# Kernel optimization log

Measured on AMD Instinct MI355X. Metric: run time of the kernel, lower is better.

## Reference

```python
import jax, jax.numpy as jnp
import numpy as np

EPS = 1e-5

def _conv(x, w, pad):
    return jax.lax.conv_general_dilated(x, w, (1, 1), pad,
        dimension_numbers=('NCHW', 'OIHW', 'NCHW'))

def _bn_relu(y, g, b):
    # training-mode BatchNorm2d: stats over (N, H, W) per channel
    mean = jnp.mean(y, axis=(0, 2, 3), keepdims=True)
    var = jnp.var(y, axis=(0, 2, 3), keepdims=True)
    yhat = (y - mean) * jax.lax.rsqrt(var + EPS)
    return jax.nn.relu(yhat * g[None, :, None, None] + b[None, :, None, None])


def setup_inputs() -> dict:
    key = jax.random.key(0)
    ks = jax.random.split(key, 12)
    B, Cin, H, W = 4, 256, 64, 64
    Ci = Cin // 4          # inter_channels = 64
    Cq = Ci // 8           # PAM q/k dim = 8
    Cout = 256
    s = 0.05
    return {
        'x':    jax.random.normal(ks[0], (B, Cin, H, W), jnp.float32),
        'w1':   jax.random.normal(ks[1], (Ci, Cin, 3, 3), jnp.float32) * s,
        'bn_g': jnp.ones((Ci,), jnp.float32),
        'bn_b': jnp.zeros((Ci,), jnp.float32),
        'wq':   jax.random.normal(ks[2], (Cq, Ci, 1, 1), jnp.float32) * s,
        'bq':   jax.random.normal(ks[3], (Cq,), jnp.float32) * s,
        'wk':   jax.random.normal(ks[4], (Cq, Ci, 1, 1), jnp.float32) * s,
        'bk':   jax.random.normal(ks[5], (Cq,), jnp.float32) * s,
        'wv':   jax.random.normal(ks[6], (Ci, Ci, 1, 1), jnp.float32) * s,
        'bv':   jax.random.normal(ks[7], (Ci,), jnp.float32) * s,
        'gamma_pam': jnp.float32(0.5) * jnp.ones((1,), jnp.float32),
        'gamma_cam': jnp.float32(0.5) * jnp.ones((1,), jnp.float32),
        'w2':   jax.random.normal(ks[8], (Ci, Ci, 3, 3), jnp.float32) * s,
        'w8':   jax.random.normal(ks[9], (Cout, Ci, 1, 1), jnp.float32) * s,
        'b8':   jax.random.normal(ks[10], (Cout,), jnp.float32) * s,
    }


def reference(x, w1, bn_g, bn_b, wq, bq, wk, bk, wv, bv,
              gamma_pam, gamma_cam, w2, w8, b8):
    B, _, H, W = x.shape
    N = H * W

    # feat1 = relu(bn1(conv1(x))); feat2 is the identical computation -> reuse
    feat1 = _bn_relu(_conv(x, w1, 'SAME'), bn_g, bn_b)   # [B, Ci, H, W]
    Ci = feat1.shape[1]

    # ---- PAM (position attention) ----
    q = _conv(feat1, wq, 'VALID') + bq[None, :, None, None]   # [B, Cq, H, W]
    k = _conv(feat1, wk, 'VALID') + bk[None, :, None, None]
    v = _conv(feat1, wv, 'VALID') + bv[None, :, None, None]   # [B, Ci, H, W]
    qf = q.reshape(B, -1, N)
    kf = k.reshape(B, -1, N)
    vf = v.reshape(B, Ci, N)
    energy = jnp.einsum('bdi,bdj->bij', qf, kf)               # [B, N, N]
    attn = jax.nn.softmax(energy, axis=-1)
    pam = jnp.einsum('bcj,bij->bci', vf, attn).reshape(B, Ci, H, W)
    sa_feat = gamma_pam[0] * pam + feat1

    sa_conv = _bn_relu(_conv(sa_feat, w2, 'SAME'), bn_g, bn_b)

    # ---- CAM (channel attention) ----
    f = feat1.reshape(B, Ci, N)
    ce = jnp.einsum('bcn,bdn->bcd', f, f)                     # [B, Ci, Ci]
    ce_new = jnp.max(ce, axis=-1, keepdims=True) - ce
    cattn = jax.nn.softmax(ce_new, axis=-1)
    cam = jnp.einsum('bcd,bdn->bcn', cattn, f).reshape(B, Ci, H, W)
    sc_feat = gamma_cam[0] * cam + feat1

    sc_conv = _bn_relu(_conv(sc_feat, w2, 'SAME'), bn_g, bn_b)

    feat_sum = sa_conv + sc_conv
    # conv8: Dropout2d (identity at inference) + 1x1 conv
    out = _conv(feat_sum, w8, 'VALID') + b8[None, :, None, None]
    return out
```

## Files before the change

### kernel.cpp

```cpp
#include <hip/hip_runtime.h>
#include <hip/hip_bf16.h>

#define BB   4
#define CIN  256
#define CI   64
#define COUT 256
#define NPIX 4096
#define LOG2E 1.44269504088896340736f

#define B_Y1V    0x0000000u
#define B_FEAT1  0x0400000u
#define B_SA     0x0800000u
#define B_Y2     0x0C00000u
#define B_SACONV 0x1000000u
#define B_Q      0x1400000u
#define B_K      0x1480000u
#define B_ST     0x15A0000u
#define B_CATT   0x15B1000u
#define B_WP1    0x15C1000u
#define B_WP2    0x1610000u
#define B_PL     0x1630000u
#define B_W8P    0x1640000u
#define B_WQKV   0x1648000u
#define B_BALL   0x164B000u

typedef __attribute__((ext_vector_type(8))) short bf16x8;
typedef __attribute__((ext_vector_type(4))) short bf16x4;
typedef __attribute__((ext_vector_type(4))) float f32x4;

__device__ __forceinline__ short f2bs(float f) {
    union { float f; unsigned u; } c; c.f = f;
    unsigned r = c.u + 0x7FFFu + ((c.u >> 16) & 1u);
    return (short)(r >> 16);
}
__device__ __forceinline__ float bs2f(unsigned short s) {
    union { unsigned u; float f; } c; c.u = ((unsigned)s) << 16;
    return c.f;
}
__device__ __forceinline__ int swz(int wp) { return (wp ^ (wp >> 2)) & 3; }


__device__ __forceinline__ void weights_body(const float* __restrict__ w1,
                                             const float* __restrict__ w2,
                                             const float* __restrict__ w8,
                                             const float* wq, const float* bq,
                                             const float* wk, const float* bk,
                                             const float* wv, const float* bv,
                                             short* wp1, short* wp2, short* w8p,
                                             short* wall, float* ball,
                                             float* st, float* pl, int blk, int t) {
    if (blk < 576) {
        int idx = blk * 256 + t;
        if (idx < 147456) {
            int cil = idx & 31, co = (idx >> 5) & 63;
            int rest = idx >> 11, tap = rest % 9, ch = rest / 9;
            wp1[idx] = f2bs(w1[co * CIN * 9 + (ch * 32 + cil) * 9 + tap]);
        }
    } else if (blk < 720) {
        int idx = (blk - 576) * 256 + t;
        if (idx < 36864) {
            int cil = idx & 31, co = (idx >> 5) & 63;
            int rest = idx >> 11, tap = rest % 9, ch = rest / 9;
            wp2[idx] = f2bs(w2[co * CI * 9 + (ch * 32 + cil) * 9 + tap]);
        }
    } else if (blk < 784) {
        int idx = (blk - 720) * 256 + t;
        w8p[idx] = f2bs(w8[idx]);
    } else if (blk < 804) {
        int idx = (blk - 784) * 256 + t;
        if (idx < 5120) {
            int co = idx >> 6, ci = idx & 63;
            float v;
            if (co < 8)       v = wq[co * 64 + ci] * LOG2E;
            else if (co < 16) v = wk[(co - 8) * 64 + ci];
            else              v = wv[(co - 16) * 64 + ci];
            wall[idx] = f2bs(v);
        }
        if (idx < 80) {
            float v;
            if (idx < 8)       v = bq[idx] * LOG2E;
            else if (idx < 16) v = bk[idx - 8];
            else               v = bv[idx - 16];
            ball[idx] = v;
        }
    } else if (blk < 806) {
        int idx = (blk - 804) * 256 + t;
        if (idx < 384) st[idx] = 0.f;
    } else {
        int idx = (blk - 806) * 256 + t;
        pl[idx] = 0.f;
    }
}

template<int NCH>
__device__ __forceinline__ void prep_body(const float* __restrict__ in,
                                          short* __restrict__ out, int blk, int t) {
    __shared__ short tl[4][64][34];
    int hq = blk & 15;
    int ch = (blk >> 4) % NCH;
    int b  = blk / (16 * NCH);
    const int CINT = NCH * 32;

    #pragma unroll
    for (int i = 0; i < 32; ++i) {
        int idx = i * 256 + t;
        int w = idx & 63, hh = (idx >> 6) & 3, ci = idx >> 8;
        float v = in[((size_t)(b * CINT + ch * 32 + ci)) * NPIX + (hq * 4 + hh) * 64 + w];
        tl[hh][w][ci] = f2bs(v);
    }
    __syncthreads();
    unsigned* outu = (unsigned*)(out + (((size_t)(b * NCH + ch)) * NPIX + hq * 4 * 64) * 32);
    #pragma unroll
    for (int i = 0; i < 16; ++i) {
        int j = i * 256 + t;
        int cip = j & 15, w = (j >> 4) & 63, hh = j >> 10;
        unsigned v = *(unsigned*)&tl[hh][w][2 * cip];
        outu[(size_t)(hh * 64 + w) * 16 + cip] = v;
    }
}

__global__ __launch_bounds__(256) void k_prepw(const float* __restrict__ x,
                                               const float* w1, const float* w2, const float* w8,
                                               const float* wq, const float* bq,
                                               const float* wk, const float* bk,
                                               const float* wv, const float* bv,
                                               short* xprep,
                                               short* wp1, short* wp2, short* w8p,
                                               short* wall, float* ball,
                                               float* st, float* pl) {
    int blk = blockIdx.x, t = threadIdx.x;
    if (blk < 512) prep_body<8>(x, xprep, blk, t);
    else weights_body(w1, w2, w8, wq, bq, wk, bk, wv, bv,
                      wp1, wp2, w8p, wall, ball, st, pl, blk - 512, t);
}

__device__ __forceinline__ void pamprep_body(const short* __restrict__ po,
                                             const float* __restrict__ pl_acc,
                                             const float* __restrict__ feat1,
                                             const float* __restrict__ gp,
                                             short* __restrict__ out, int blk, int t) {
    __shared__ short tl[4][64][34];
    int hq = blk & 15;
    int ch = (blk >> 4) & 1;
    int b  = blk >> 5;
    float g = gp[0];

    #pragma unroll
    for (int i = 0; i < 32; ++i) {
        int idx = i * 256 + t;
        int w = idx & 63, hh = (idx >> 6) & 3, ci = idx >> 8;
        int pix = (hq * 4 + hh) * 64 + w;
        size_t o = ((size_t)(b * 64 + ch * 32 + ci)) * NPIX + pix;
        float s = bs2f((unsigned short)po[o])
                + bs2f((unsigned short)po[o + 1048576])
                + bs2f((unsigned short)po[o + 2097152])
                + bs2f((unsigned short)po[o + 3145728]);
        float v = feat1[o] + g * s / pl_acc[b * NPIX + pix];
        tl[hh][w][ci] = f2bs(v);
    }
    __syncthreads();
    unsigned* outu = (unsigned*)(out + (((size_t)(b * 2 + ch)) * NPIX + hq * 4 * 64) * 32);
    #pragma unroll
    for (int i = 0; i < 16; ++i) {
        int j = i * 256 + t;
        int cip = j & 15, w = (j >> 4) & 63, hh = j >> 10;
        unsigned v = *(unsigned*)&tl[hh][w][2 * cip];
        outu[(size_t)(hh * 64 + w) * 16 + cip] = v;
    }
}

__global__ __launch_bounds__(256) void k_preppam(const float* __restrict__ scfeat,
                                                 short* __restrict__ sprep_sc,
                                                 const short* __restrict__ po,
                                                 const float* __restrict__ pl_acc,
                                                 const float* __restrict__ feat1,
                                                 const float* __restrict__ gp,
                                                 short* __restrict__ saprep) {
    int blk = blockIdx.x, t = threadIdx.x;
    if (blk < 128) prep_body<2>(scfeat, sprep_sc, blk, t);
    else pamprep_body(po, pl_acc, feat1, gp, saprep, blk - 128, t);
}

template<int NCH>
__device__ __forceinline__ void conv_body(const short* __restrict__ xprep,
                                          const short* __restrict__ wp,
                                          float* __restrict__ y0,
                                          float* __restrict__ y1,
                                          int blk, int t) {
    __shared__ __align__(16) short xl[3][66][32];
    int lane = t & 63, wv = t >> 6;
    int ks = blk >> 8;
    int b = (blk >> 6) & 3, h = blk & 63;
    int g = lane >> 4, n16 = lane & 15;
    constexpr int NH = NCH / 2;
    int c0 = ks * NH;

    if (t < 24) {
        int r = t >> 3, cc = ((t >> 2) & 1) ? 65 : 0, u = t & 3;
        bf16x8 z = {};
        *(bf16x8*)&xl[r][cc][u * 8] = z;
    }

    f32x4 acc[4];
    #pragma unroll
    for (int i = 0; i < 4; ++i) acc[i] = (f32x4){0.f, 0.f, 0.f, 0.f};

    int sw = t >> 2, su = t & 3;
    int spu = su ^ swz(sw + 1);

    for (int ch = c0; ch < c0 + NH; ++ch) {
        __syncthreads();
        #pragma unroll
        for (int r = 0; r < 3; ++r) {
            int hh = h + r - 1;
            bf16x8 v = {};
            if (hh >= 0 && hh < 64)
                v = *(const bf16x8*)(xprep + (((size_t)(b * NCH + ch)) * 64 + hh) * 64 * 32 + sw * 32 + su * 8);
            *(bf16x8*)&xl[r][sw + 1][spu * 8] = v;
        }
        __syncthreads();

        const short* wbase = wp + ((size_t)(ch * 9)) * 64 * 32;
        #pragma unroll
        for (int tap = 0; tap < 9; ++tap) {
            int kr = tap / 3, kc = tap % 3;
            bf16x8 a = *(const bf16x8*)(wbase + ((size_t)(tap * 64 + wv * 16 + n16)) * 32 + g * 8);
            #pragma unroll
            for (int nt = 0; nt < 4; ++nt) {
                int wpix = nt * 16 + n16 + kc;
                int pu = g ^ swz(wpix);
                bf16x8 bx = *(const bf16x8*)&xl[kr][wpix][pu * 8];
                acc[nt] = __builtin_amdgcn_mfma_f32_16x16x32_bf16(a, bx, acc[nt], 0, 0, 0);
            }
        }
    }

    float* y = ks ? y1 : y0;
    #pragma unroll
    for (int nt = 0; nt < 4; ++nt) {
        #pragma unroll
        for (int r = 0; r < 4; ++r) {
            int co = wv * 16 + g * 4 + r;
            y[((size_t)(b * CI + co)) * NPIX + h * 64 + nt * 16 + n16] = acc[nt][r];
        }
    }
}

template<int NCH>
__global__ __launch_bounds__(256) void k_convmfma(const short* __restrict__ xprep,
                                                  const short* __restrict__ wp,
                                                  float* __restrict__ y0,
                                                  float* __restrict__ y1) {
    conv_body<NCH>(xprep, wp, y0, y1, blockIdx.x, threadIdx.x);
}

__global__ __launch_bounds__(256) void k_conv2x(const short* __restrict__ inA,
                                                const short* __restrict__ inB,
                                                const short* __restrict__ wp,
                                                float* a0, float* a1,
                                                float* b0, float* b1) {
    int blk = blockIdx.x;
    int w = blk >> 9;
    conv_body<2>(w ? inB : inA, wp, w ? b0 : a0, w ? b1 : a1, blk & 511, threadIdx.x);
}

__device__ __forceinline__ void bnstats_body(const float* __restrict__ y0,
                                             const float* __restrict__ y1,
                                             float* stats, int blk, int t) {
    int c = blk >> 2, b = blk & 3;
    size_t base = ((size_t)(b * 64 + c)) * NPIX;
    float s = 0.f, sq = 0.f;
    for (int i = t; i < NPIX; i += 256) {
        float v = y0[base + i] + y1[base + i];
        s += v; sq += v * v;
    }
    __shared__ float rs[8];
    for (int o = 32; o; o >>= 1) { s += __shfl_down(s, o); sq += __shfl_down(sq, o); }
    if ((t & 63) == 0) { rs[t >> 6] = s; rs[4 + (t >> 6)] = sq; }
    __syncthreads();
    if (t == 0) {
        atomicAdd(&stats[c], rs[0] + rs[1] + rs[2] + rs[3]);
        atomicAdd(&stats[64 + c], rs[4] + rs[5] + rs[6] + rs[7]);
    }
}

__global__ __launch_bounds__(256) void k_bnstats(const float* y0, const float* y1, float* stats) {
    bnstats_body(y0, y1, stats, blockIdx.x, threadIdx.x);
}
__global__ __launch_bounds__(256) void k_bnstats2x(const float* a0, const float* a1,
                                                   const float* b0, const float* b1,
                                                   float* sta, float* stb) {
    int blk = blockIdx.x;
    int w = blk >> 8;
    bnstats_body(w ? b0 : a0, w ? b1 : a1, w ? stb : sta, blk & 255, threadIdx.x);
}

__device__ __forceinline__ void bnapply_body(const float* y0, const float* y1,
                                             const float* stats, const float* g,
                                             const float* bta, float* out, int i) {
    int c = (i >> 12) & 63;
    float mean = stats[c] * (1.f / 16384.f);
    float var = stats[64 + c] * (1.f / 16384.f) - mean * mean;
    float rs = rsqrtf(var + 1e-5f);
    float v = (y0[i] + y1[i] - mean) * rs * g[c] + bta[c];
    out[i] = v > 0.f ? v : 0.f;
}

__global__ __launch_bounds__(256) void k_bnapply2(const float* y0, const float* y1,
                                                  const float* stats, const float* g,
                                                  const float* bta, float* out) {
    bnapply_body(y0, y1, stats, g, bta, out, blockIdx.x * 256 + threadIdx.x);
}
__global__ __launch_bounds__(256) void k_bnapply2x(const float* a0, const float* a1,
                                                   const float* b0, const float* b1,
                                                   const float* sta, const float* stb,
                                                   const float* g, const float* bta,
                                                   float* oa, float* ob) {
    int blk = blockIdx.x;
    int w = blk >> 12;
    int i = (blk & 4095) * 256 + threadIdx.x;
    bnapply_body(w ? b0 : a0, w ? b1 : a1, w ? stb : sta, g, bta, w ? ob : oa, i);
}

__device__ __forceinline__ void qkv_body(const float* __restrict__ feat1,
                                         const short* __restrict__ wall,
                                         const float* __restrict__ ball,
                                         short* __restrict__ q,
                                         short* __restrict__ k,
                                         short* __restrict__ v, int blk, int t) {
    __shared__ __align__(16) short fl[64][64];
    int lane = t & 63, wv = t >> 6;
    int h = blk & 63, b = blk >> 6;
    int n16 = lane & 15, g = lane >> 4;

    {
        int n = t & 63, ug2 = t >> 6;
        const float* fp = feat1 + ((size_t)b * CI) * NPIX + h * 64 + n;
        #pragma unroll
        for (int uu = 0; uu < 2; ++uu) {
            int u = ug2 + uu * 4;
            int ci0 = u * 8;
            short tmp[8];
            #pragma unroll
            for (int j = 0; j < 8; ++j) tmp[j] = f2bs(fp[(size_t)(ci0 + j) * NPIX]);
            int phys = u ^ (n & 7);
            *(bf16x8*)&fl[n][phys * 8] = *(bf16x8*)tmp;
        }
    }
    __syncthreads();

    f32x4 acc[4];
    #pragma unroll
    for (int i = 0; i < 4; ++i) acc[i] = (f32x4){0.f, 0.f, 0.f, 0.f};
    f32x4 acc4 = (f32x4){0.f, 0.f, 0.f, 0.f};

    #pragma unroll
    for (int kc = 0; kc < 2; ++kc) {
        bf16x8 a = *(const bf16x8*)&wall[(size_t)(wv * 16 + n16) * 64 + kc * 32 + g * 8];
        bf16x8 a4 = *(const bf16x8*)&wall[(size_t)(64 + n16) * 64 + kc * 32 + g * 8];
        #pragma unroll
        for (int nt = 0; nt < 4; ++nt) {
            int n = nt * 16 + n16;
            int phys = (kc * 4 + g) ^ (n & 7);
            bf16x8 bx = *(const bf16x8*)&fl[n][phys * 8];
            acc[nt] = __builtin_amdgcn_mfma_f32_16x16x32_bf16(a, bx, acc[nt], 0, 0, 0);
            if (nt == wv) acc4 = __builtin_amdgcn_mfma_f32_16x16x32_bf16(a4, bx, acc4, 0, 0, 0);
        }
    }

    #pragma unroll
    for (int nt = 0; nt < 4; ++nt) {
        int pix = h * 64 + nt * 16 + n16;
        #pragma unroll
        for (int r = 0; r < 4; ++r) {
            int co = wv * 16 + g * 4 + r;
            short val = f2bs(acc[nt][r] + ball[co]);
            if (co < 8)       q[((size_t)(b * 8 + co)) * NPIX + pix] = val;
            else if (co < 16) k[((size_t)(b * 8 + co - 8)) * NPIX + pix] = val;
            else              v[((size_t)(b * 64 + co - 16)) * NPIX + pix] = val;
        }
    }
    {
        int pix = h * 64 + wv * 16 + n16;
        #pragma unroll
        for (int r = 0; r < 4; ++r) {
            int co = 64 + g * 4 + r;
            v[((size_t)(b * 64 + co - 16)) * NPIX + pix] = f2bs(acc4[r] + ball[co]);
        }
    }
}

__device__ __forceinline__ void gram_body(const float* __restrict__ f,
                                          float* __restrict__ gp, int blk, int t) {
    __shared__ __align__(16) float fl[64 * 68];
    int b = blk >> 6, nc = blk & 63;
    int n0 = nc * 64;
    int c = t & 63, dg = t >> 6;
    float acc[16];
    #pragma unroll
    for (int i = 0; i < 16; ++i) acc[i] = 0.f;
    for (int idx = t; idx < 4096; idx += 256) {
        int cc = idx >> 6, nn = idx & 63;
        fl[nn * 68 + cc] = f[((size_t)b * 64 + cc) * NPIX + n0 + nn];
    }
    __syncthreads();
    for (int nn = 0; nn < 64; ++nn) {
        float fc = fl[nn * 68 + c];
        const float4* fd = (const float4*)(fl + nn * 68 + dg * 16);
        #pragma unroll
        for (int k4 = 0; k4 < 4; ++k4) {
            float4 vv = fd[k4];
            acc[k4 * 4 + 0] += fc * vv.x;
            acc[k4 * 4 + 1] += fc * vv.y;
            acc[k4 * 4 + 2] += fc * vv.z;
            acc[k4 * 4 + 3] += fc * vv.w;
        }
    }
    float* dst = gp + (size_t)nc * 16384 + ((size_t)b * 64 + c) * 64 + dg * 16;
    #pragma unroll
    for (int kk = 0; kk < 16; ++kk) dst[kk] = acc[kk];
}

__global__ __launch_bounds__(256) void k_qkvgram(const float* __restrict__ feat1,
                                                 const short* __restrict__ wall,
                                                 const float* __restrict__ ball,
                                                 short* q, short* k, short* v,
                                                 float* gp) {
    int blk = blockIdx.x, t = threadIdx.x;
    if (blk < 256) qkv_body(feat1, wall, ball, q, k, v, blk, t);
    else gram_body(feat1, gp, blk - 256, t);
}

__global__ __launch_bounds__(256) void k_pampart(const short* __restrict__ q,
                                                 const short* __restrict__ k,
                                                 const short* __restrict__ v,
                                                 short* __restrict__ po,
                                                 float* __restrict__ pl_acc) {
    __shared__ short kl[128][20];
    __shared__ __align__(16) short pl[64][128];

    int t = threadIdx.x;
    int lane = t & 63, w = t >> 6;
    int blk = blockIdx.x;
    int jc = blk >> 8, b = (blk >> 6) & 3, ic = blk & 63;
    int i0 = ic * 64;
    int n16 = lane & 15, g = lane >> 4;
    int key = n16 & 7;

    const short* qb = q + (size_t)b * 8 * NPIX;
    const short* kb = k + (size_t)b * 8 * NPIX;
    const short* vb = v + (size_t)b * 64 * NPIX;

    #pragma unroll
    for (int i = 0; i < 2; ++i) {
        int idx = i * 256 + t;
        int jj = idx & 127, dz = 8 + ((idx >> 7) << 1);
        *(unsigned*)&kl[jj][dz] = 0u;
    }

    bf16x8 aq = {};
    if (lane < 16) {
        int irow = i0 + w * 16 + lane;
        #pragma unroll
        for (int e = 0; e < 8; ++e) aq[e] = qb[(size_t)e * NPIX + irow];
    }

    f32x4 acc[4];
    #pragma unroll
    for (int i = 0; i < 4; ++i) acc[i] = (f32x4){0.f, 0.f, 0.f, 0.f};
    float lacc = 0.f;
    const f32x4 zz = {0.f, 0.f, 0.f, 0.f};

    for (int ro = 0; ro < 8; ++ro) {
        int j0 = jc * 1024 + ro * 128;
        #pragma unroll
        for (int i = 0; i < 2; ++i) {
            int idx = i * 256 + t;
            int jj = idx & 127, dp2 = idx >> 7;
            unsigned lo = (unsigned short)kb[(size_t)(dp2 * 2) * NPIX + j0 + jj];
            unsigned hi = (unsigned short)kb[(size_t)(dp2 * 2 + 1) * NPIX + j0 + jj];
            *(unsigned*)&kl[jj][dp2 * 2] = lo | (hi << 16);
        }
        bf16x8 av[4];
        #pragma unroll
        for (int ks = 0; ks < 4; ++ks)
            av[ks] = *(const bf16x8*)&vb[(size_t)(w * 16 + n16) * NPIX + j0 + ks * 32 + g * 8];
        __syncthreads();

        __builtin_amdgcn_s_setprio(1);
        #pragma unroll
        for (int jsub = 0; jsub < 8; ++jsub) {
            bf16x8 bk = {};
            if (lane < 32) {
                bf16x4 lo = *(const bf16x4*)&kl[jsub * 16 + n16][g * 8];
                bf16x4 hi = *(const bf16x4*)&kl[jsub * 16 + n16][g * 8 + 4];
                bk = __builtin_shufflevector(lo, hi, 0, 1, 2, 3, 4, 5, 6, 7);
            }
            f32x4 s = __builtin_amdgcn_mfma_f32_16x16x32_bf16(bk, aq, zz, 0, 0, 0);
            float e0 = exp2f(s[0]), e1 = exp2f(s[1]), e2 = exp2f(s[2]), e3 = exp2f(s[3]);
            lacc += (e0 + e1) + (e2 + e3);
            bf16x4 pk = { f2bs(e0), f2bs(e1), f2bs(e2), f2bs(e3) };
            int uw = (jsub * 2 + (g >> 1)) ^ key;
            *(bf16x4*)&pl[w * 16 + n16][uw * 8 + (g & 1) * 4] = pk;
        }
        __builtin_amdgcn_s_setprio(0);
        __syncthreads();

        __builtin_amdgcn_s_setprio(1);
        #pragma unroll
        for (int isub = 0; isub < 4; ++isub) {
            #pragma unroll
            for (int ks = 0; ks < 4; ++ks) {
                int ur = (ks * 4 + g) ^ key;
                bf16x8 bp = *(const bf16x8*)&pl[isub * 16 + n16][ur * 8];
                acc[isub] = __builtin_amdgcn_mfma_f32_16x16x32_bf16(av[ks], bp, acc[isub], 0, 0, 0);
            }
        }
        __builtin_amdgcn_s_setprio(0);
        __syncthreads();
    }

    {
        float lv = lacc;
        lv += __shfl_xor(lv, 16);
        lv += __shfl_xor(lv, 32);
        if (lane < 16)
            atomicAdd(&pl_acc[b * NPIX + i0 + w * 16 + lane], lv);
    }

    #pragma unroll
    for (int isub = 0; isub < 4; ++isub) {
        #pragma unroll
        for (int r = 0; r < 4; ++r) {
            int c = w * 16 + g * 4 + r;
            size_t o = ((size_t)((jc * BB + b) * 64 + c)) * NPIX + i0 + isub * 16 + n16;
            po[o] = f2bs(acc[isub][r]);
        }
    }
}

__global__ void k_camsm2(const float* __restrict__ gp, float* __restrict__ cattn) {
    int row = blockIdx.x;
    int d = threadIdx.x;
    float v = 0.f;
    #pragma unroll 8
    for (int p = 0; p < 64; ++p) v += gp[(size_t)p * 16384 + row * 64 + d];
    float mn = v;
    for (int s = 32; s; s >>= 1) mn = fminf(mn, __shfl_xor(mn, s));
    float e = exp2f((mn - v) * LOG2E);
    float sum = e;
    for (int s = 32; s; s >>= 1) sum += __shfl_xor(sum, s);
    cattn[(size_t)row * 64 + d] = e / sum;
}

__global__ __launch_bounds__(256) void k_cam(const float* __restrict__ cattn,
                                             const float* __restrict__ f,
                                             const float* __restrict__ gcp,
                                             float* __restrict__ sc) {
    __shared__ __align__(16) float Al[64 * 68];
    __shared__ float fl[64 * 64];
    int blk = blockIdx.x;
    int b = blk >> 6, nc = blk & 63;
    int n0 = nc * 64;
    int t = threadIdx.x;
    int nl = t & 63, cg = t >> 6;
    for (int idx = t; idx < 4096; idx += 256) {
        int cc = idx >> 6, dd = idx & 63;
        Al[dd * 68 + cc] = cattn[((size_t)b * 64 + cc) * 64 + dd];
    }
    for (int idx = t; idx < 4096; idx += 256) {
        int dd = idx >> 6, nn = idx & 63;
        fl[dd * 64 + nn] = f[((size_t)b * 64 + dd) * NPIX + n0 + nn];
    }
    __syncthreads();
    float acc[16];
    #pragma unroll
    for (int i = 0; i < 16; ++i) acc[i] = 0.f;
    for (int d = 0; d < 64; ++d) {
        float fv = fl[d * 64 + nl];
        const float4* A4 = (const float4*)(Al + d * 68 + cg * 16);
        #pragma unroll
        for (int k4 = 0; k4 < 4; ++k4) {
            float4 a = A4[k4];
            acc[k4 * 4 + 0] += a.x * fv;
            acc[k4 * 4 + 1] += a.y * fv;
            acc[k4 * 4 + 2] += a.z * fv;
            acc[k4 * 4 + 3] += a.w * fv;
        }
    }
    float g = gcp[0];
    #pragma unroll
    for (int kk = 0; kk < 16; ++kk) {
        int c = cg * 16 + kk;
        size_t o = ((size_t)b * 64 + c) * NPIX + n0 + nl;
        sc[o] = g * acc[kk] + f[o];
    }
}

__global__ __launch_bounds__(256) void k_finalmfma(const float* __restrict__ sa,
                                                   const float* __restrict__ sc,
                                                   const short* __restrict__ w8p,
                                                   const float* __restrict__ b8,
                                                   float* __restrict__ out) {
    __shared__ __align__(16) short fl[64][64];
    int t = threadIdx.x;
    int lane = t & 63, wv = t >> 6;
    int blk = blockIdx.x;
    int h = blk & 63, b = (blk >> 6) & 3, cq = blk >> 8;
    int n16 = lane & 15, g = lane >> 4;

    {
        int n = t & 63, ug2 = t >> 6;
        const float* sap = sa + ((size_t)b * CI) * NPIX + h * 64 + n;
        const float* scp = sc + ((size_t)b * CI) * NPIX + h * 64 + n;
        #pragma unroll
        for (int uu = 0; uu < 2; ++uu) {
            int u = ug2 + uu * 4;
            int ci0 = u * 8;
            short tmp[8];
            #pragma unroll
            for (int j = 0; j < 8; ++j) {
                size_t o = (size_t)(ci0 + j) * NPIX;
                tmp[j] = f2bs(sap[o] + scp[o]);
            }
            int phys = u ^ (n & 7);
            *(bf16x8*)&fl[n][phys * 8] = *(bf16x8*)tmp;
        }
    }
    __syncthreads();

    f32x4 acc[4];
    #pragma unroll
    for (int i = 0; i < 4; ++i) acc[i] = (f32x4){0.f, 0.f, 0.f, 0.f};
    int cobase = cq * 64 + wv * 16;

    #pragma unroll
    for (int kc = 0; kc < 2; ++kc) {
        bf16x8 a = *(const bf16x8*)&w8p[(size_t)(cobase + n16) * 64 + kc * 32 + g * 8];
        #pragma unroll
        for (int nt = 0; nt < 4; ++nt) {
            int n = nt * 16 + n16;
            int phys = (kc * 4 + g) ^ (n & 7);
            bf16x8 bx = *(const bf16x8*)&fl[n][phys * 8];
            acc[nt] = __builtin_amdgcn_mfma_f32_16x16x32_bf16(a, bx, acc[nt], 0, 0, 0);
        }
    }

    #pragma unroll
    for (int nt = 0; nt < 4; ++nt) {
        #pragma unroll
        for (int r = 0; r < 4; ++r) {
            int co = cobase + g * 4 + r;
            out[((size_t)(b * COUT + co)) * NPIX + h * 64 + nt * 16 + n16] = acc[nt][r] + b8[co];
        }
    }
}

extern "C" void kernel_launch(void* const* d_in, const int* in_sizes, int n_in,
                              void* d_out, int out_size, void* d_ws, size_t ws_size,
                              hipStream_t stream) {
    (void)in_sizes; (void)n_in; (void)out_size; (void)ws_size;
    const float* x    = (const float*)d_in[0];
    const float* w1   = (const float*)d_in[1];
    const float* bng  = (const float*)d_in[2];
    const float* bnb  = (const float*)d_in[3];
    const float* wq   = (const float*)d_in[4];
    const float* bq   = (const float*)d_in[5];
    const float* wk   = (const float*)d_in[6];
    const float* bk   = (const float*)d_in[7];
    const float* wv   = (const float*)d_in[8];
    const float* bv   = (const float*)d_in[9];
    const float* gpam = (const float*)d_in[10];
    const float* gcam = (const float*)d_in[11];
    const float* w2   = (const float*)d_in[12];
    const float* w8   = (const float*)d_in[13];
    const float* b8   = (const float*)d_in[14];
    float* out = (float*)d_out;

    char* WB = (char*)d_ws;
    float* fC1P0   = (float*)(WB + B_Y1V);
    float* fC1P1   = (float*)(WB + B_SACONV);
    float* fGP     = (float*)(WB + B_SACONV);
    short* fV      = (short*)(WB + B_Y1V);
    short* fSPREPSC= (short*)(WB + B_Y1V + 0x200000);
    short* fSAPREP = (short*)(WB + B_Y1V);
    float* fFEAT1  = (float*)(WB + B_FEAT1);
    short* fXPREP  = (short*)(WB + B_SA);
    float* fSCFEAT = (float*)(WB + B_SA);
    float* fC2B1   = (float*)(WB + B_SA);
    short* fPO     = (short*)(WB + B_Y2);
    float* fC2A0   = (float*)(WB + B_Y2);
    float* fC2B0   = (float*)(WB + B_FEAT1);
    float* fC2A1   = (float*)(WB + B_SACONV);
    short* fQ      = (short*)(WB + B_Q);
    short* fK      = (short*)(WB + B_K);
    float* fST     = (float*)(WB + B_ST);
    float* fST2a   = fST + 128;
    float* fST2b   = fST + 256;
    float* fCATT   = (float*)(WB + B_CATT);
    short* fWP1    = (short*)(WB + B_WP1);
    short* fWP2    = (short*)(WB + B_WP2);
    float* fPL     = (float*)(WB + B_PL);
    short* fW8P    = (short*)(WB + B_W8P);
    short* fWQKV   = (short*)(WB + B_WQKV);
    float* fBALL   = (float*)(WB + B_BALL);

    k_prepw<<<1382, 256, 0, stream>>>(x, w1, w2, w8, wq, bq, wk, bk, wv, bv,
                                      fXPREP, fWP1, fWP2, fW8P, fWQKV, fBALL, fST, fPL);

    k_convmfma<8><<<512, 256, 0, stream>>>(fXPREP, fWP1, fC1P0, fC1P1);
    k_bnstats<<<256, 256, 0, stream>>>(fC1P0, fC1P1, fST);
    k_bnapply2<<<4096, 256, 0, stream>>>(fC1P0, fC1P1, fST, bng, bnb, fFEAT1);

    k_qkvgram<<<512, 256, 0, stream>>>(fFEAT1, fWQKV, fBALL, fQ, fK, fV, fGP);
    k_camsm2<<<256, 64, 0, stream>>>(fGP, fCATT);

    k_pampart<<<1024, 256, 0, stream>>>(fQ, fK, fV, fPO, fPL);
    k_cam<<<256, 256, 0, stream>>>(fCATT, fFEAT1, gcam, fSCFEAT);
    k_preppam<<<256, 256, 0, stream>>>(fSCFEAT, fSPREPSC, fPO, fPL, fFEAT1, gpam, fSAPREP);

    k_conv2x<<<1024, 256, 0, stream>>>(fSAPREP, fSPREPSC, fWP2, fC2A0, fC2A1, fC2B0, fC2B1);
    k_bnstats2x<<<512, 256, 0, stream>>>(fC2A0, fC2A1, fC2B0, fC2B1, fST2a, fST2b);
    k_bnapply2x<<<8192, 256, 0, stream>>>(fC2A0, fC2A1, fC2B0, fC2B1, fST2a, fST2b,
                                          bng, bnb, fC2A1, fC2B1);

    k_finalmfma<<<1024, 256, 0, stream>>>(fC2A1, fC2B1, fW8P, b8, out);
}
```

Baseline: 136.4 us.

## Fuse CAM matmul with bf16 conv-input prep and split BN stats across more blocks

The CAM attention product now writes the gamma-scaled residual directly in the packed bf16 layout that the second conv consumes. It is merged into one launch with the PAM prep, which removes the fp32 sc_feat round trip and one kernel launch. Separately, the BN statistics kernels split each channel/batch plane into four chunks, giving four times as many blocks. The cost is four times as many atomic adds, plus a change in the floating-point summation order.

```diff
diff --git a/kernel.cpp b/kernel.cpp
--- a/kernel.cpp
+++ b/kernel.cpp
@@ -169,16 +169,61 @@
     }
 }
 
-__global__ __launch_bounds__(256) void k_preppam(const float* __restrict__ scfeat,
-                                                 short* __restrict__ sprep_sc,
-                                                 const short* __restrict__ po,
-                                                 const float* __restrict__ pl_acc,
-                                                 const float* __restrict__ feat1,
-                                                 const float* __restrict__ gp,
-                                                 short* __restrict__ saprep) {
+__device__ __forceinline__ void camprep_body(const float* __restrict__ cattn,
+                                             const float* __restrict__ f,
+                                             const float* __restrict__ gcp,
+                                             short* __restrict__ out, int blk, int t) {
+    __shared__ __align__(16) float Al[64 * 68];
+    __shared__ float fl[64 * 64];
+    int b = blk >> 6, nc = blk & 63;
+    int n0 = nc * 64;
+    int nl = t & 63, cg = t >> 6;
+    for (int idx = t; idx < 4096; idx += 256) {
+        int cc = idx >> 6, dd = idx & 63;
+        Al[dd * 68 + cc] = cattn[((size_t)b * 64 + cc) * 64 + dd];
+    }
+    for (int idx = t; idx < 4096; idx += 256) {
+        int dd = idx >> 6, nn = idx & 63;
+        fl[dd * 64 + nn] = f[((size_t)b * 64 + dd) * NPIX + n0 + nn];
+    }
+    __syncthreads();
+    float acc[16];
+    #pragma unroll
+    for (int i = 0; i < 16; ++i) acc[i] = 0.f;
+    for (int d = 0; d < 64; ++d) {
+        float fv = fl[d * 64 + nl];
+        const float4* A4 = (const float4*)(Al + d * 68 + cg * 16);
+        #pragma unroll
+        for (int k4 = 0; k4 < 4; ++k4) {
+            float4 a = A4[k4];
+            acc[k4 * 4 + 0] += a.x * fv;
+            acc[k4 * 4 + 1] += a.y * fv;
+            acc[k4 * 4 + 2] += a.z * fv;
+            acc[k4 * 4 + 3] += a.w * fv;
+        }
+    }
+    float g = gcp[0];
+    int pix = n0 + nl;
+    unsigned* du = (unsigned*)out + ((size_t)(b * 2 + (cg >> 1)) * NPIX + pix) * 16 + (cg & 1) * 8;
+    #pragma unroll
+    for (int m = 0; m < 8; ++m) {
+        float v0 = g * acc[2 * m]     + fl[(cg * 16 + 2 * m) * 64 + nl];
+        float v1 = g * acc[2 * m + 1] + fl[(cg * 16 + 2 * m + 1) * 64 + nl];
+        du[m] = (unsigned)(unsigned short)f2bs(v0) | ((unsigned)(unsigned short)f2bs(v1) << 16);
+    }
+}
+
+__global__ __launch_bounds__(256) void k_campam(const float* __restrict__ cattn,
+                                                const float* __restrict__ feat1,
+                                                const float* __restrict__ gcp,
+                                                short* __restrict__ sprep_sc,
+                                                const short* __restrict__ po,
+                                                const float* __restrict__ pl_acc,
+                                                const float* __restrict__ gpam,
+                                                short* __restrict__ saprep) {
     int blk = blockIdx.x, t = threadIdx.x;
-    if (blk < 128) prep_body<2>(scfeat, sprep_sc, blk, t);
-    else pamprep_body(po, pl_acc, feat1, gp, saprep, blk - 128, t);
+    if (blk < 256) camprep_body(cattn, feat1, gcp, sprep_sc, blk, t);
+    else pamprep_body(po, pl_acc, feat1, gpam, saprep, blk - 256, t);
 }
 
 template<int NCH>
@@ -267,11 +312,14 @@
 __device__ __forceinline__ void bnstats_body(const float* __restrict__ y0,
                                              const float* __restrict__ y1,
                                              float* stats, int blk, int t) {
-    int c = blk >> 2, b = blk & 3;
-    size_t base = ((size_t)(b * 64 + c)) * NPIX;
+    int pc = blk & 3;
+    int cb = blk >> 2;
+    int c = cb >> 2, b = cb & 3;
+    size_t base = ((size_t)(b * 64 + c)) * NPIX + pc * 1024;
     float s = 0.f, sq = 0.f;
-    for (int i = t; i < NPIX; i += 256) {
-        float v = y0[base + i] + y1[base + i];
+    #pragma unroll
+    for (int i = 0; i < 4; ++i) {
+        float v = y0[base + i * 256 + t] + y1[base + i * 256 + t];
         s += v; sq += v * v;
     }
     __shared__ float rs[8];
@@ -291,8 +339,8 @@
                                                    const float* b0, const float* b1,
                                                    float* sta, float* stb) {
     int blk = blockIdx.x;
-    int w = blk >> 8;
-    bnstats_body(w ? b0 : a0, w ? b1 : a1, w ? stb : sta, blk & 255, threadIdx.x);
+    int w = blk >> 10;
+    bnstats_body(w ? b0 : a0, w ? b1 : a1, w ? stb : sta, blk & 1023, threadIdx.x);
 }
 
 __device__ __forceinline__ void bnapply_body(const float* y0, const float* y1,
@@ -551,50 +599,6 @@
     float sum = e;
     for (int s = 32; s; s >>= 1) sum += __shfl_xor(sum, s);
     cattn[(size_t)row * 64 + d] = e / sum;
-}
-
-__global__ __launch_bounds__(256) void k_cam(const float* __restrict__ cattn,
-                                             const float* __restrict__ f,
-                                             const float* __restrict__ gcp,
-                                             float* __restrict__ sc) {
-    __shared__ __align__(16) float Al[64 * 68];
-    __shared__ float fl[64 * 64];
-    int blk = blockIdx.x;
-    int b = blk >> 6, nc = blk & 63;
-    int n0 = nc * 64;
-    int t = threadIdx.x;
-    int nl = t & 63, cg = t >> 6;
-    for (int idx = t; idx < 4096; idx += 256) {
-        int cc = idx >> 6, dd = idx & 63;
-        Al[dd * 68 + cc] = cattn[((size_t)b * 64 + cc) * 64 + dd];
-    }
-    for (int idx = t; idx < 4096; idx += 256) {
-        int dd = idx >> 6, nn = idx & 63;
-        fl[dd * 64 + nn] = f[((size_t)b * 64 + dd) * NPIX + n0 + nn];
-    }
-    __syncthreads();
-    float acc[16];
-    #pragma unroll
-    for (int i = 0; i < 16; ++i) acc[i] = 0.f;
-    for (int d = 0; d < 64; ++d) {
-        float fv = fl[d * 64 + nl];
-        const float4* A4 = (const float4*)(Al + d * 68 + cg * 16);
-        #pragma unroll
-        for (int k4 = 0; k4 < 4; ++k4) {
-            float4 a = A4[k4];
-            acc[k4 * 4 + 0] += a.x * fv;
-            acc[k4 * 4 + 1] += a.y * fv;
-            acc[k4 * 4 + 2] += a.z * fv;
-            acc[k4 * 4 + 3] += a.w * fv;
-        }
-    }
-    float g = gcp[0];
-    #pragma unroll
-    for (int kk = 0; kk < 16; ++kk) {
-        int c = cg * 16 + kk;
-        size_t o = ((size_t)b * 64 + c) * NPIX + n0 + nl;
-        sc[o] = g * acc[kk] + f[o];
-    }
 }
 
 __global__ __launch_bounds__(256) void k_finalmfma(const float* __restrict__ sa,
@@ -686,7 +690,6 @@
     short* fSAPREP = (short*)(WB + B_Y1V);
     float* fFEAT1  = (float*)(WB + B_FEAT1);
     short* fXPREP  = (short*)(WB + B_SA);
-    float* fSCFEAT = (float*)(WB + B_SA);
     float* fC2B1   = (float*)(WB + B_SA);
     short* fPO     = (short*)(WB + B_Y2);
     float* fC2A0   = (float*)(WB + B_Y2);
@@ -709,18 +712,17 @@
                                       fXPREP, fWP1, fWP2, fW8P, fWQKV, fBALL, fST, fPL);
 
     k_convmfma<8><<<512, 256, 0, stream>>>(fXPREP, fWP1, fC1P0, fC1P1);
-    k_bnstats<<<256, 256, 0, stream>>>(fC1P0, fC1P1, fST);
+    k_bnstats<<<1024, 256, 0, stream>>>(fC1P0, fC1P1, fST);
     k_bnapply2<<<4096, 256, 0, stream>>>(fC1P0, fC1P1, fST, bng, bnb, fFEAT1);
 
     k_qkvgram<<<512, 256, 0, stream>>>(fFEAT1, fWQKV, fBALL, fQ, fK, fV, fGP);
     k_camsm2<<<256, 64, 0, stream>>>(fGP, fCATT);
 
     k_pampart<<<1024, 256, 0, stream>>>(fQ, fK, fV, fPO, fPL);
-    k_cam<<<256, 256, 0, stream>>>(fCATT, fFEAT1, gcam, fSCFEAT);
-    k_preppam<<<256, 256, 0, stream>>>(fSCFEAT, fSPREPSC, fPO, fPL, fFEAT1, gpam, fSAPREP);
+    k_campam<<<384, 256, 0, stream>>>(fCATT, fFEAT1, gcam, fSPREPSC, fPO, fPL, gpam, fSAPREP);
 
     k_conv2x<<<1024, 256, 0, stream>>>(fSAPREP, fSPREPSC, fWP2, fC2A0, fC2A1, fC2B0, fC2B1);
-    k_bnstats2x<<<512, 256, 0, stream>>>(fC2A0, fC2A1, fC2B0, fC2B1, fST2a, fST2b);
+    k_bnstats2x<<<2048, 256, 0, stream>>>(fC2A0, fC2A1, fC2B0, fC2B1, fST2a, fST2b);
     k_bnapply2x<<<8192, 256, 0, stream>>>(fC2A0, fC2A1, fC2B0, fC2B1, fST2a, fST2b,
                                           bng, bnb, fC2A1, fC2B1);
 
```

Result: no change. 135.1 us (-0.9%).
